# Performance work log

Measured on AMD Instinct MI355X. Metric: run time of the kernel, lower is better.

The kernel has to match this reference:

```python
import jax, jax.numpy as jnp
import numpy as np

S = 4          # number of species / per-species sub-modules
CUTOFF = 5.2


def _routed_mlp(feat, W, b, species_, activate=True):
    # Species-routed MLP: equivalent to per-species index_select -> m_i -> index_add.
    # Compute all species branches vectorized, then select with one-hot mask.
    h = jnp.einsum('ni,sio->nso', feat, W) + b            # [N, S, out]
    if activate:
        h = jax.nn.gelu(h)
    onehot = jax.nn.one_hot(species_, S, dtype=feat.dtype)  # [N, S]; -1 -> all-zero row
    return jnp.einsum('nso,ns->no', h, onehot)            # [N, out]


def _smooth_cutoff(d, rc):
    x = jnp.clip(d / rc, 0.0, 1.0 - 1e-6)
    f = jnp.exp(1.0 - 1.0 / (1.0 - x * x))
    return jnp.where(d < rc, f, 0.0)


def setup_inputs() -> dict:
    key = jax.random.key(0)
    ks = jax.random.split(key, 12)
    B, A, AEV, MO, NO, P = 256, 128, 1008, 256, 128, 262144
    N = B * A
    FIN = MO + NO  # 384
    species = jax.random.randint(ks[0], (B, A), 0, S, dtype=jnp.int32)
    aev = jax.random.normal(ks[1], (B, A, AEV), dtype=jnp.float32)
    atom_index12 = jax.random.randint(ks[2], (2, P), 0, N, dtype=jnp.int32)
    distances = jax.random.uniform(ks[3], (P,), dtype=jnp.float32) * CUTOFF
    total_charges = jax.random.randint(ks[4], (B,), -2, 3).astype(jnp.float32)

    def w(k, shape, fan_in):
        return jax.random.normal(k, shape, dtype=jnp.float32) / np.sqrt(fan_in)

    Wm0 = w(ks[5], (S, AEV, MO), AEV); bm0 = jnp.zeros((S, MO), jnp.float32)
    Wn0 = w(ks[6], (S, MO, NO), MO);   bn0 = jnp.zeros((S, NO), jnp.float32)
    Wm1 = w(ks[7], (S, FIN, MO), FIN); bm1 = jnp.zeros((S, MO), jnp.float32)
    Wn1 = w(ks[8], (S, MO, NO), MO);   bn1 = jnp.zeros((S, NO), jnp.float32)
    Wf  = w(ks[9], (S, FIN, 1), FIN);  bf  = jnp.zeros((S, 1), jnp.float32)
    return dict(species=species, aev=aev, atom_index12=atom_index12,
                distances=distances, total_charges=total_charges,
                Wm0=Wm0, bm0=bm0, Wn0=Wn0, bn0=bn0,
                Wm1=Wm1, bm1=bm1, Wn1=Wn1, bn1=bn1,
                Wf=Wf, bf=bf,
                factor=jnp.float32(1.0), prefactor=jnp.float32(1.0))


def reference(species, aev, atom_index12, distances, total_charges,
              Wm0, bm0, Wn0, bn0, Wm1, bm1, Wn1, bn1, Wf, bf,
              factor, prefactor):
    B, A = species.shape
    species_ = species.reshape(-1)                 # [N]
    feat = aev.reshape(-1, aev.shape[-1])          # [N, AEV]

    # ExpDistanceDecay * smooth cutoff, shared by every pass
    decay = (prefactor ** 2) * jnp.exp(-(factor ** 2) * distances) \
            * _smooth_cutoff(distances, CUTOFF)    # [P]
    idx_flat = atom_index12.reshape(-1)            # [2P] scatter targets
    idx_flip = atom_index12[::-1].reshape(-1)      # [2P] gather sources (flipud)
    decay2 = jnp.tile(decay, 2)                    # [2P]

    for (Wm, bm, Wn, bn) in ((Wm0, bm0, Wn0, bn0), (Wm1, bm1, Wn1, bn1)):
        internal = _routed_mlp(feat, Wm, bm, species_)     # [N, MO]
        neigh = _routed_mlp(internal, Wn, bn, species_)    # [N, NO]
        msgs = neigh[idx_flip] * decay2[:, None]           # [2P, NO]
        merged = jnp.zeros_like(neigh).at[idx_flat].add(msgs)
        feat = jnp.concatenate([internal, merged], axis=-1)  # [N, MO+NO]

    pre = _routed_mlp(feat, Wf, bf, species_, activate=False)[:, 0].reshape(B, A)

    dummy_mask = species != -1
    n_real = dummy_mask.sum(-1, keepdims=True).astype(pre.dtype)
    charges = pre + (total_charges - pre.sum(-1))[:, None] / n_real
    charges = jnp.where(dummy_mask, charges, 0.0)
    return species, charges, pre
```

## Files before the change

kernel.cpp:

```cpp
#include <hip/hip_runtime.h>
#include <hip/hip_bf16.h>
#include <math.h>

constexpr int S_  = 4;
constexpr int MO  = 256;
constexpr int NO  = 128;
constexpr int FIN = 384;
#define CUTOFF_F 5.2f

typedef short bf16x8 __attribute__((ext_vector_type(8)));
typedef float f32x16 __attribute__((ext_vector_type(16)));

__device__ __forceinline__ float gelu_tanh(float x) {
    float u = 0.7978845608028654f * (x + 0.044715f * x * x * x);
    return 0.5f * x * (1.0f + tanhf(u));
}
__device__ __forceinline__ unsigned short f2bf(float x) {
    unsigned u = __float_as_uint(x);
    u = (u + 0x7fffu + ((u >> 16) & 1u)) >> 16;
    return (unsigned short)u;
}
__device__ __forceinline__ float bf2f(unsigned short h) {
    return __uint_as_float(((unsigned)h) << 16);
}

__global__ void decay_kernel(const float* __restrict__ dist, const float* __restrict__ fa_,
                             const float* __restrict__ pf_, float* __restrict__ decay, int P) {
    int i = blockIdx.x * blockDim.x + threadIdx.x;
    if (i >= P) return;
    float fa = fa_[0], pf = pf_[0];
    float d = dist[i];
    float x = fminf(fmaxf(d / CUTOFF_F, 0.0f), 1.0f - 1e-6f);
    float f = expf(1.0f - 1.0f / (1.0f - x * x));
    float w = (d < CUTOFF_F) ? f : 0.0f;
    decay[i] = pf * pf * expf(-(fa * fa) * d) * w;
}

__global__ void species_hist(const int* __restrict__ sp, int* __restrict__ bhist, int N) {
    __shared__ int h[S_];
    int t = threadIdx.x, b = blockIdx.x;
    if (t < S_) h[t] = 0;
    __syncthreads();
    int i = b * 256 + t;
    if (i < N) {
        int s = sp[i];
        if (s >= 0 && s < S_) atomicAdd(&h[s], 1);
    }
    __syncthreads();
    if (t < S_) bhist[b * 4 + t] = h[t];
}
__global__ void species_scan(const int* __restrict__ bhist, int* __restrict__ cnt,
                             int* __restrict__ pbase, int nb) {
    if (threadIdx.x != 0) return;
    int tot[S_];
    for (int s = 0; s < S_; ++s) {
        int sum = 0;
        for (int b = 0; b < nb; ++b) sum += bhist[b * 4 + s];
        tot[s] = sum;
    }
    int off = 0;
    for (int s = 0; s < S_; ++s) { cnt[s] = tot[s]; cnt[4 + s] = off; off += tot[s]; }
    for (int s = 0; s < S_; ++s) {
        int run = cnt[4 + s];
        for (int b = 0; b < nb; ++b) { pbase[b * 4 + s] = run; run += bhist[b * 4 + s]; }
    }
}
__global__ void species_fill(const int* __restrict__ sp, const int* __restrict__ pbase,
                             int* __restrict__ perm, int N) {
    __shared__ int cur[S_];
    int t = threadIdx.x, b = blockIdx.x;
    if (t < S_) cur[t] = pbase[b * 4 + t];
    __syncthreads();
    int i = b * 256 + t;
    if (i < N) {
        int s = sp[i];
        if (s >= 0 && s < S_) {
            int pos = atomicAdd(&cur[s], 1);
            perm[pos] = i;
        }
    }
}

__global__ void edge_count(const int* __restrict__ ai, int* __restrict__ degree, int P2) {
    int e = blockIdx.x * blockDim.x + threadIdx.x;
    if (e < P2) atomicAdd(&degree[ai[e]], 1);
}
__global__ void scan_rowptr(const int* __restrict__ degree, int* __restrict__ rowptr,
                            int* __restrict__ cursor, int N) {
    __shared__ int lds[1024];
    int t = threadIdx.x;
    int per = N / 1024;
    int base = t * per;
    int sum = 0;
    for (int i = 0; i < per; ++i) sum += degree[base + i];
    lds[t] = sum;
    __syncthreads();
    int v = sum;
    for (int ofs = 1; ofs < 1024; ofs <<= 1) {
        int add = (t >= ofs) ? lds[t - ofs] : 0;
        __syncthreads();
        v += add;
        lds[t] = v;
        __syncthreads();
    }
    int run = v - sum;
    for (int i = 0; i < per; ++i) {
        int d = degree[base + i];
        rowptr[base + i] = run;
        cursor[base + i] = run;
        run += d;
    }
    if (t == 1023) rowptr[N] = run;
}
__global__ void edge_fill(const int* __restrict__ ai, const float* __restrict__ decay,
                          int* __restrict__ cursor, int* __restrict__ col,
                          float* __restrict__ wgt, int P) {
    int e = blockIdx.x * blockDim.x + threadIdx.x;
    if (e >= 2 * P) return;
    int p = (e < P) ? e : e - P;
    int dst = ai[e];
    int src = (e < P) ? ai[P + p] : ai[p];
    int pos = atomicAdd(&cursor[dst], 1);
    col[pos] = src;
    wgt[pos] = decay[p];
}

__global__ void cast_aev(const float* __restrict__ in, unsigned short* __restrict__ outb, int total4) {
    int i = blockIdx.x * blockDim.x + threadIdx.x;
    if (i >= total4) return;
    float4 v = ((const float4*)in)[i];
    ushort4 o; o.x = f2bf(v.x); o.y = f2bf(v.y); o.z = f2bf(v.z); o.w = f2bf(v.w);
    ((ushort4*)outb)[i] = o;
}

__global__ void transpose_cast(const float* __restrict__ W, unsigned short* __restrict__ Wt,
                               int K, int NC) {
    __shared__ float tile[32][33];
    int s = blockIdx.z;
    int nb = blockIdx.x * 32, kb = blockIdx.y * 32;
    int tx = threadIdx.x & 31, ty = threadIdx.x >> 5;
    const float* Wb = W + (size_t)s * K * NC;
    unsigned short* Wo = Wt + (size_t)s * NC * K;
#pragma unroll
    for (int i = 0; i < 4; ++i) {
        int k = kb + ty + i * 8;
        tile[ty + i * 8][tx] = (k < K) ? Wb[(size_t)k * NC + nb + tx] : 0.0f;
    }
    __syncthreads();
#pragma unroll
    for (int i = 0; i < 4; ++i) {
        int n = nb + ty + i * 8;
        int k = kb + tx;
        if (k < K) Wo[(size_t)n * K + k] = f2bf(tile[tx][ty + i * 8]);
    }
}

template<int K, int NC, bool ACT>
__launch_bounds__(256, 2)
__global__ void mfma_gemm(const unsigned short* __restrict__ A, int lda,
                          const unsigned short* __restrict__ Wt,
                          const float* __restrict__ bias,
                          unsigned short* __restrict__ C, int ldc,
                          const int* __restrict__ cnt, const int* __restrict__ perm) {
    const int s = blockIdx.z;
    const int count = cnt[s];
    const int row0 = blockIdx.y * 128;
    if (row0 >= count) return;
    const int off = cnt[4 + s];
    const int c0 = blockIdx.x * 128;

    __shared__ unsigned short As[128 * 40];
    __shared__ unsigned short Bs[128 * 40];
    __shared__ int rix[128];

    const int t = threadIdx.x;
    const int lane = t & 63, wave = t >> 6;
    const int wm = wave >> 1, wn = wave & 1;
    const int l31 = lane & 31, lhi = lane >> 5;

    if (t < 128) {
        int ri = row0 + t;
        rix[t] = (ri < count) ? perm[off + ri] : -1;
    }
    __syncthreads();

    const int r2 = t >> 1, half = t & 1;
    const int gA = rix[r2];
    const unsigned short* wrow = Wt + ((size_t)s * NC + c0 + r2) * K;

    f32x16 acc00 = {}, acc01 = {}, acc10 = {}, acc11 = {};
    const float4 zf4 = make_float4(0.f, 0.f, 0.f, 0.f);

    for (int k0 = 0; k0 < K; k0 += 32) {
        const int kk = k0 + half * 16;
        const bool v = (kk < K);
        float4 a0 = zf4, a1 = zf4, b0 = zf4, b1 = zf4;
        if (v) {
            if (gA >= 0) {
                const float4* p = (const float4*)(A + (size_t)gA * lda + kk);
                a0 = p[0]; a1 = p[1];
            }
            const float4* q = (const float4*)(wrow + kk);
            b0 = q[0]; b1 = q[1];
        }
        __syncthreads();
        *(float4*)(&As[r2 * 40 + half * 16])     = a0;
        *(float4*)(&As[r2 * 40 + half * 16 + 8]) = a1;
        *(float4*)(&Bs[r2 * 40 + half * 16])     = b0;
        *(float4*)(&Bs[r2 * 40 + half * 16 + 8]) = b1;
        __syncthreads();
#pragma unroll
        for (int ks = 0; ks < 2; ++ks) {
            const int ch = (ks * 2 + lhi) * 8;
            bf16x8 fa0 = *(const bf16x8*)(&As[(wm * 64 +  0 + l31) * 40 + ch]);
            bf16x8 fa1 = *(const bf16x8*)(&As[(wm * 64 + 32 + l31) * 40 + ch]);
            bf16x8 fb0 = *(const bf16x8*)(&Bs[(wn * 64 +  0 + l31) * 40 + ch]);
            bf16x8 fb1 = *(const bf16x8*)(&Bs[(wn * 64 + 32 + l31) * 40 + ch]);
            acc00 = __builtin_amdgcn_mfma_f32_32x32x16_bf16(fa0, fb0, acc00, 0, 0, 0);
            acc01 = __builtin_amdgcn_mfma_f32_32x32x16_bf16(fa0, fb1, acc01, 0, 0, 0);
            acc10 = __builtin_amdgcn_mfma_f32_32x32x16_bf16(fa1, fb0, acc10, 0, 0, 0);
            acc11 = __builtin_amdgcn_mfma_f32_32x32x16_bf16(fa1, fb1, acc11, 0, 0, 0);
        }
    }

    const float* bp = bias + s * NC;
    auto store = [&](const f32x16& vv, int fm, int fn) {
        int col = c0 + wn * 64 + fn * 32 + l31;
        float bia = bp[col];
#pragma unroll
        for (int reg = 0; reg < 16; ++reg) {
            int frow = (reg & 3) + 8 * (reg >> 2) + 4 * lhi;
            int r = wm * 64 + fm * 32 + frow;
            int g = rix[r];
            if (g >= 0) {
                float x = vv[reg] + bia;
                if (ACT) x = gelu_tanh(x);
                C[(size_t)g * ldc + col] = f2bf(x);
            }
        }
    };
    store(acc00, 0, 0); store(acc01, 0, 1); store(acc10, 1, 0); store(acc11, 1, 1);
}

template<int MODE>
__global__ void gather_rows(const unsigned short* __restrict__ neigh,
                            const int* __restrict__ rowptr, const int* __restrict__ col,
                            const float* __restrict__ wgt,
                            unsigned short* __restrict__ featout,
                            float* __restrict__ mergedout) {
    int row = blockIdx.x * 4 + (threadIdx.x >> 6);
    int lane = threadIdx.x & 63;
    int b = rowptr[row], e = rowptr[row + 1];
    int j = lane * 2;
    float a0 = 0.f, a1 = 0.f;
    for (int i = b; i < e; ++i) {
        int src = col[i];
        float w = wgt[i];
        unsigned pk = *(const unsigned*)(neigh + (size_t)src * NO + j);
        a0 += bf2f((unsigned short)(pk & 0xffffu)) * w;
        a1 += bf2f((unsigned short)(pk >> 16)) * w;
    }
    if (MODE == 0) {
        unsigned short o0 = f2bf(a0), o1 = f2bf(a1);
        *(unsigned*)(featout + (size_t)row * FIN + MO + j) = ((unsigned)o1 << 16) | (unsigned)o0;
    } else {
        float2 o; o.x = a0; o.y = a1;
        *(float2*)(mergedout + (size_t)row * NO + j) = o;
    }
}

__global__ void final_kernel(const unsigned short* __restrict__ int1, const float* __restrict__ merged,
                             const float* __restrict__ Wf, const float* __restrict__ bfb,
                             const int* __restrict__ species, float* __restrict__ out, int N) {
    int w = (int)((blockIdx.x * (size_t)blockDim.x + threadIdx.x) >> 6);
    int lane = threadIdx.x & 63;
    if (w >= N) return;
    int s = species[w];
    float acc = 0.0f;
    if (s >= 0) {
        const float* wp = Wf + (size_t)s * FIN;
        for (int k = lane; k < MO; k += 64) acc += bf2f(int1[(size_t)w * MO + k]) * wp[k];
        for (int k = lane; k < NO; k += 64) acc += merged[(size_t)w * NO + k] * wp[MO + k];
    }
    for (int o = 32; o > 0; o >>= 1) acc += __shfl_down(acc, o, 64);
    if (lane == 0) {
        float pre = (s >= 0) ? (acc + bfb[s]) : 0.0f;
        out[2 * (size_t)N + w] = pre;
        out[w] = (float)s;
    }
}

__global__ void charges_kernel(const float* __restrict__ pre_buf, const int* __restrict__ species,
                               const float* __restrict__ tc, float* __restrict__ out, int N, int A) {
    int b = blockIdx.x;
    int a = threadIdx.x;
    int idx = b * A + a;
    float pre = pre_buf[idx];
    int sp = species[idx];
    bool mask = (sp != -1);
    float v = pre;
    int c = mask ? 1 : 0;
    for (int o = 32; o > 0; o >>= 1) {
        v += __shfl_down(v, o, 64);
        c += __shfl_down(c, o, 64);
    }
    __shared__ float ssum[2];
    __shared__ int scnt[2];
    int wid = threadIdx.x >> 6;
    if ((threadIdx.x & 63) == 0) { ssum[wid] = v; scnt[wid] = c; }
    __syncthreads();
    float total = ssum[0] + ssum[1];
    int nreal = scnt[0] + scnt[1];
    float ch = pre + (tc[b] - total) / (float)max(nreal, 1);
    out[(size_t)N + idx] = mask ? ch : 0.0f;
}

extern "C" void kernel_launch(void* const* d_in, const int* in_sizes, int n_in,
                              void* d_out, int out_size, void* d_ws, size_t ws_size,
                              hipStream_t stream) {
    const int*   species = (const int*)d_in[0];
    const float* aev     = (const float*)d_in[1];
    const int*   ai      = (const int*)d_in[2];
    const float* dist    = (const float*)d_in[3];
    const float* tc      = (const float*)d_in[4];
    const float* Wm0 = (const float*)d_in[5];  const float* bm0 = (const float*)d_in[6];
    const float* Wn0 = (const float*)d_in[7];  const float* bn0 = (const float*)d_in[8];
    const float* Wm1 = (const float*)d_in[9];  const float* bm1 = (const float*)d_in[10];
    const float* Wn1 = (const float*)d_in[11]; const float* bn1 = (const float*)d_in[12];
    const float* Wf  = (const float*)d_in[13]; const float* bf  = (const float*)d_in[14];
    const float* factor    = (const float*)d_in[15];
    const float* prefactor = (const float*)d_in[16];

    const int N   = in_sizes[0];
    const int AEV = in_sizes[1] / N;
    const int P   = in_sizes[3];
    const int B   = in_sizes[4];
    const int A   = N / B;

    float* out = (float*)d_out;

    char* base = (char*)d_ws;
    size_t o = 0;
    auto take = [&](size_t bytes) -> char* {
        o = (o + 255) & ~(size_t)255;
        char* p = base + o; o += bytes; return p;
    };
    unsigned short* feat1_bf = (unsigned short*)take((size_t)N * FIN * 2);
    unsigned short* int1_bf  = (unsigned short*)take((size_t)N * MO * 2);
    char* region             = take((size_t)N * AEV * 2);
    unsigned short* aev_bf   = (unsigned short*)region;
    unsigned short* neigh_bf = (unsigned short*)region;
    size_t roff = ((size_t)N * NO * 2 + 255) & ~(size_t)255;
    float* merged_f = (float*)(region + roff);
    roff += (size_t)N * NO * 4;
    roff = (roff + 255) & ~(size_t)255;
    int* rowptr = (int*)(region + roff);  roff += (size_t)(N + 1) * 4; roff = (roff + 255) & ~(size_t)255;
    int* cursor = (int*)(region + roff);  roff += (size_t)N * 4;       roff = (roff + 255) & ~(size_t)255;
    int* degree = (int*)(region + roff);  roff += (size_t)N * 4;       roff = (roff + 255) & ~(size_t)255;
    int* ecol   = (int*)(region + roff);  roff += (size_t)2 * P * 4;   roff = (roff + 255) & ~(size_t)255;
    float* ewgt = (float*)(region + roff);
    float* decay = (float*)take((size_t)P * 4);
    unsigned short* Wm0t = (unsigned short*)take((size_t)S_ * MO * AEV * 2);
    unsigned short* Wn0t = (unsigned short*)take((size_t)S_ * NO * MO * 2);
    unsigned short* Wm1t = (unsigned short*)take((size_t)S_ * MO * FIN * 2);
    unsigned short* Wn1t = (unsigned short*)take((size_t)S_ * NO * MO * 2);
    int* perm  = (int*)take((size_t)N * 4);
    int* cnt   = (int*)take(64);
    const int nb = (N + 255) / 256;
    int* bhist = (int*)take((size_t)nb * 4 * 4);
    int* pbase = (int*)take((size_t)nb * 4 * 4);

    species_hist<<<nb, 256, 0, stream>>>(species, bhist, N);
    species_scan<<<1, 64, 0, stream>>>(bhist, cnt, pbase, nb);
    species_fill<<<nb, 256, 0, stream>>>(species, pbase, perm, N);
    decay_kernel<<<(P + 255) / 256, 256, 0, stream>>>(dist, factor, prefactor, decay, P);

    const int tot4 = N * (AEV / 4);
    cast_aev<<<(tot4 + 255) / 256, 256, 0, stream>>>(aev, aev_bf, tot4);
    transpose_cast<<<dim3(MO / 32, (AEV + 31) / 32, S_), 256, 0, stream>>>(Wm0, Wm0t, AEV, MO);
    transpose_cast<<<dim3(NO / 32, MO / 32, S_), 256, 0, stream>>>(Wn0, Wn0t, MO, NO);
    transpose_cast<<<dim3(MO / 32, FIN / 32, S_), 256, 0, stream>>>(Wm1, Wm1t, FIN, MO);
    transpose_cast<<<dim3(NO / 32, MO / 32, S_), 256, 0, stream>>>(Wn1, Wn1t, MO, NO);

    const int rb = (N + 127) / 128;

    mfma_gemm<1008, 256, true><<<dim3(2, rb, S_), 256, 0, stream>>>(
        aev_bf, AEV, Wm0t, bm0, feat1_bf, FIN, cnt, perm);

    hipMemsetAsync(degree, 0, (size_t)N * 4, stream);
    edge_count<<<(2 * P + 255) / 256, 256, 0, stream>>>(ai, degree, 2 * P);
    scan_rowptr<<<1, 1024, 0, stream>>>(degree, rowptr, cursor, N);
    edge_fill<<<(2 * P + 255) / 256, 256, 0, stream>>>(ai, decay, cursor, ecol, ewgt, P);

    mfma_gemm<256, 128, true><<<dim3(1, rb, S_), 256, 0, stream>>>(
        feat1_bf, FIN, Wn0t, bn0, neigh_bf, NO, cnt, perm);
    gather_rows<0><<<N / 4, 256, 0, stream>>>(neigh_bf, rowptr, ecol, ewgt, feat1_bf, nullptr);

    mfma_gemm<384, 256, true><<<dim3(2, rb, S_), 256, 0, stream>>>(
        feat1_bf, FIN, Wm1t, bm1, int1_bf, MO, cnt, perm);
    mfma_gemm<256, 128, true><<<dim3(1, rb, S_), 256, 0, stream>>>(
        int1_bf, MO, Wn1t, bn1, neigh_bf, NO, cnt, perm);
    gather_rows<1><<<N / 4, 256, 0, stream>>>(neigh_bf, rowptr, ecol, ewgt, nullptr, merged_f);

    final_kernel<<<(N * 64 + 255) / 256, 256, 0, stream>>>(
        int1_bf, merged_f, Wf, bf, species, out, N);
    charges_kernel<<<B, A, 0, stream>>>(out + 2 * (size_t)N, species, tc, out, N, A);
}
```

Measured before the change: 724.1 us.

## Fuse fp32 AEV cast into first GEMM and double-buffer shared tiles

```diff
diff --git a/kernel.cpp b/kernel.cpp
--- a/kernel.cpp
+++ b/kernel.cpp
@@ -125,14 +125,6 @@
     wgt[pos] = decay[p];
 }
 
-__global__ void cast_aev(const float* __restrict__ in, unsigned short* __restrict__ outb, int total4) {
-    int i = blockIdx.x * blockDim.x + threadIdx.x;
-    if (i >= total4) return;
-    float4 v = ((const float4*)in)[i];
-    ushort4 o; o.x = f2bf(v.x); o.y = f2bf(v.y); o.z = f2bf(v.z); o.w = f2bf(v.w);
-    ((ushort4*)outb)[i] = o;
-}
-
 __global__ void transpose_cast(const float* __restrict__ W, unsigned short* __restrict__ Wt,
                                int K, int NC) {
     __shared__ float tile[32][33];
@@ -155,9 +147,9 @@
     }
 }
 
-template<int K, int NC, bool ACT>
+template<int K, int NC, bool ACT, bool AF32>
 __launch_bounds__(256, 2)
-__global__ void mfma_gemm(const unsigned short* __restrict__ A, int lda,
+__global__ void mfma_gemm(const void* __restrict__ Aptr, int lda,
                           const unsigned short* __restrict__ Wt,
                           const float* __restrict__ bias,
                           unsigned short* __restrict__ C, int ldc,
@@ -169,8 +161,8 @@
     const int off = cnt[4 + s];
     const int c0 = blockIdx.x * 128;
 
-    __shared__ unsigned short As[128 * 40];
-    __shared__ unsigned short Bs[128 * 40];
+    __shared__ unsigned short As[2][128 * 40];
+    __shared__ unsigned short Bs[2][128 * 40];
     __shared__ int rix[128];
 
     const int t = threadIdx.x;
@@ -189,38 +181,79 @@
     const unsigned short* wrow = Wt + ((size_t)s * NC + c0 + r2) * K;
 
     f32x16 acc00 = {}, acc01 = {}, acc10 = {}, acc11 = {};
-    const float4 zf4 = make_float4(0.f, 0.f, 0.f, 0.f);
-
-    for (int k0 = 0; k0 < K; k0 += 32) {
-        const int kk = k0 + half * 16;
+
+    uint4 pa0 = {0,0,0,0}, pa1 = {0,0,0,0}, pb0 = {0,0,0,0}, pb1 = {0,0,0,0};
+    float4 fa0{}, fa1{}, fa2{}, fa3{};
+
+    auto prefetch = [&](int it) {
+        const int kk = it * 32 + half * 16;
         const bool v = (kk < K);
-        float4 a0 = zf4, a1 = zf4, b0 = zf4, b1 = zf4;
+        uint4 z = {0,0,0,0};
+        pb0 = z; pb1 = z;
         if (v) {
-            if (gA >= 0) {
-                const float4* p = (const float4*)(A + (size_t)gA * lda + kk);
-                a0 = p[0]; a1 = p[1];
+            const uint4* q = (const uint4*)(wrow + kk);
+            pb0 = q[0]; pb1 = q[1];
+        }
+        if (AF32) {
+            float4 zf = make_float4(0.f,0.f,0.f,0.f);
+            fa0 = zf; fa1 = zf; fa2 = zf; fa3 = zf;
+            if (v && gA >= 0) {
+                const float4* p = (const float4*)((const float*)Aptr + (size_t)gA * lda + kk);
+                fa0 = p[0]; fa1 = p[1]; fa2 = p[2]; fa3 = p[3];
             }
-            const float4* q = (const float4*)(wrow + kk);
-            b0 = q[0]; b1 = q[1];
-        }
+        } else {
+            pa0 = z; pa1 = z;
+            if (v && gA >= 0) {
+                const uint4* p = (const uint4*)((const unsigned short*)Aptr + (size_t)gA * lda + kk);
+                pa0 = p[0]; pa1 = p[1];
+            }
+        }
+    };
+    auto stage = [&](int buf) {
+        uint4 aw0, aw1;
+        if (AF32) {
+            union { unsigned short us[8]; uint4 v; } k0, k1;
+            const float* f0 = (const float*)&fa0;
+            const float* f1 = (const float*)&fa1;
+            const float* f2 = (const float*)&fa2;
+            const float* f3 = (const float*)&fa3;
+#pragma unroll
+            for (int i = 0; i < 4; ++i) { k0.us[i] = f2bf(f0[i]); k0.us[4 + i] = f2bf(f1[i]); }
+#pragma unroll
+            for (int i = 0; i < 4; ++i) { k1.us[i] = f2bf(f2[i]); k1.us[4 + i] = f2bf(f3[i]); }
+            aw0 = k0.v; aw1 = k1.v;
+        } else {
+            aw0 = pa0; aw1 = pa1;
+        }
+        *(uint4*)(&As[buf][r2 * 40 + half * 16])     = aw0;
+        *(uint4*)(&As[buf][r2 * 40 + half * 16 + 8]) = aw1;
+        *(uint4*)(&Bs[buf][r2 * 40 + half * 16])     = pb0;
+        *(uint4*)(&Bs[buf][r2 * 40 + half * 16 + 8]) = pb1;
+    };
+
+    const int NIT = (K + 31) / 32;
+    prefetch(0);
+    stage(0);
+    int cur = 0;
+
+    for (int it = 0; it < NIT; ++it) {
         __syncthreads();
-        *(float4*)(&As[r2 * 40 + half * 16])     = a0;
-        *(float4*)(&As[r2 * 40 + half * 16 + 8]) = a1;
-        *(float4*)(&Bs[r2 * 40 + half * 16])     = b0;
-        *(float4*)(&Bs[r2 * 40 + half * 16 + 8]) = b1;
-        __syncthreads();
+        const bool more = (it + 1 < NIT);
+        if (more) prefetch(it + 1);
 #pragma unroll
         for (int ks = 0; ks < 2; ++ks) {
             const int ch = (ks * 2 + lhi) * 8;
-            bf16x8 fa0 = *(const bf16x8*)(&As[(wm * 64 +  0 + l31) * 40 + ch]);
-            bf16x8 fa1 = *(const bf16x8*)(&As[(wm * 64 + 32 + l31) * 40 + ch]);
-            bf16x8 fb0 = *(const bf16x8*)(&Bs[(wn * 64 +  0 + l31) * 40 + ch]);
-            bf16x8 fb1 = *(const bf16x8*)(&Bs[(wn * 64 + 32 + l31) * 40 + ch]);
-            acc00 = __builtin_amdgcn_mfma_f32_32x32x16_bf16(fa0, fb0, acc00, 0, 0, 0);
-            acc01 = __builtin_amdgcn_mfma_f32_32x32x16_bf16(fa0, fb1, acc01, 0, 0, 0);
-            acc10 = __builtin_amdgcn_mfma_f32_32x32x16_bf16(fa1, fb0, acc10, 0, 0, 0);
-            acc11 = __builtin_amdgcn_mfma_f32_32x32x16_bf16(fa1, fb1, acc11, 0, 0, 0);
-        }
+            bf16x8 a0 = *(const bf16x8*)(&As[cur][(wm * 64 +  0 + l31) * 40 + ch]);
+            bf16x8 a1 = *(const bf16x8*)(&As[cur][(wm * 64 + 32 + l31) * 40 + ch]);
+            bf16x8 b0 = *(const bf16x8*)(&Bs[cur][(wn * 64 +  0 + l31) * 40 + ch]);
+            bf16x8 b1 = *(const bf16x8*)(&Bs[cur][(wn * 64 + 32 + l31) * 40 + ch]);
+            acc00 = __builtin_amdgcn_mfma_f32_32x32x16_bf16(a0, b0, acc00, 0, 0, 0);
+            acc01 = __builtin_amdgcn_mfma_f32_32x32x16_bf16(a0, b1, acc01, 0, 0, 0);
+            acc10 = __builtin_amdgcn_mfma_f32_32x32x16_bf16(a1, b0, acc10, 0, 0, 0);
+            acc11 = __builtin_amdgcn_mfma_f32_32x32x16_bf16(a1, b1, acc11, 0, 0, 0);
+        }
+        if (more) stage(cur ^ 1);
+        cur ^= 1;
     }
 
     const float* bp = bias + s * NC;
@@ -348,7 +381,6 @@
     unsigned short* feat1_bf = (unsigned short*)take((size_t)N * FIN * 2);
     unsigned short* int1_bf  = (unsigned short*)take((size_t)N * MO * 2);
     char* region             = take((size_t)N * AEV * 2);
-    unsigned short* aev_bf   = (unsigned short*)region;
     unsigned short* neigh_bf = (unsigned short*)region;
     size_t roff = ((size_t)N * NO * 2 + 255) & ~(size_t)255;
     float* merged_f = (float*)(region + roff);
@@ -375,8 +407,11 @@
     species_fill<<<nb, 256, 0, stream>>>(species, pbase, perm, N);
     decay_kernel<<<(P + 255) / 256, 256, 0, stream>>>(dist, factor, prefactor, decay, P);
 
-    const int tot4 = N * (AEV / 4);
-    cast_aev<<<(tot4 + 255) / 256, 256, 0, stream>>>(aev, aev_bf, tot4);
+    hipMemsetAsync(degree, 0, (size_t)N * 4, stream);
+    edge_count<<<(2 * P + 255) / 256, 256, 0, stream>>>(ai, degree, 2 * P);
+    scan_rowptr<<<1, 1024, 0, stream>>>(degree, rowptr, cursor, N);
+    edge_fill<<<(2 * P + 255) / 256, 256, 0, stream>>>(ai, decay, cursor, ecol, ewgt, P);
+
     transpose_cast<<<dim3(MO / 32, (AEV + 31) / 32, S_), 256, 0, stream>>>(Wm0, Wm0t, AEV, MO);
     transpose_cast<<<dim3(NO / 32, MO / 32, S_), 256, 0, stream>>>(Wn0, Wn0t, MO, NO);
     transpose_cast<<<dim3(MO / 32, FIN / 32, S_), 256, 0, stream>>>(Wm1, Wm1t, FIN, MO);
@@ -384,21 +419,15 @@
 
     const int rb = (N + 127) / 128;
 
-    mfma_gemm<1008, 256, true><<<dim3(2, rb, S_), 256, 0, stream>>>(
-        aev_bf, AEV, Wm0t, bm0, feat1_bf, FIN, cnt, perm);
-
-    hipMemsetAsync(degree, 0, (size_t)N * 4, stream);
-    edge_count<<<(2 * P + 255) / 256, 256, 0, stream>>>(ai, degree, 2 * P);
-    scan_rowptr<<<1, 1024, 0, stream>>>(degree, rowptr, cursor, N);
-    edge_fill<<<(2 * P + 255) / 256, 256, 0, stream>>>(ai, decay, cursor, ecol, ewgt, P);
-
-    mfma_gemm<256, 128, true><<<dim3(1, rb, S_), 256, 0, stream>>>(
+    mfma_gemm<1008, 256, true, true><<<dim3(2, rb, S_), 256, 0, stream>>>(
+        aev, AEV, Wm0t, bm0, feat1_bf, FIN, cnt, perm);
+    mfma_gemm<256, 128, true, false><<<dim3(1, rb, S_), 256, 0, stream>>>(
         feat1_bf, FIN, Wn0t, bn0, neigh_bf, NO, cnt, perm);
     gather_rows<0><<<N / 4, 256, 0, stream>>>(neigh_bf, rowptr, ecol, ewgt, feat1_bf, nullptr);
 
-    mfma_gemm<384, 256, true><<<dim3(2, rb, S_), 256, 0, stream>>>(
+    mfma_gemm<384, 256, true, false><<<dim3(2, rb, S_), 256, 0, stream>>>(
         feat1_bf, FIN, Wm1t, bm1, int1_bf, MO, cnt, perm);
-    mfma_gemm<256, 128, true><<<dim3(1, rb, S_), 256, 0, stream>>>(
+    mfma_gemm<256, 128, true, false><<<dim3(1, rb, S_), 256, 0, stream>>>(
         int1_bf, MO, Wn1t, bn1, neigh_bf, NO, cnt, perm);
     gather_rows<1><<<N / 4, 256, 0, stream>>>(neigh_bf, rowptr, ecol, ewgt, nullptr, merged_f);
 
```

After: 691.2 us. -4.5%, faster.

## Double-buffer LDS tiles with register prefetch and widen K step in MFMA GEMM

Applied to the files above, without the earlier changes.

```diff
diff --git a/kernel.cpp b/kernel.cpp
--- a/kernel.cpp
+++ b/kernel.cpp
@@ -154,6 +154,8 @@
         if (k < K) Wo[(size_t)n * K + k] = f2bf(tile[tx][ty + i * 8]);
     }
 }
+
+constexpr int LSTR = 72;
 
 template<int K, int NC, bool ACT>
 __launch_bounds__(256, 2)
@@ -169,8 +171,8 @@
     const int off = cnt[4 + s];
     const int c0 = blockIdx.x * 128;
 
-    __shared__ unsigned short As[128 * 40];
-    __shared__ unsigned short Bs[128 * 40];
+    __shared__ unsigned short As[2][128 * LSTR];
+    __shared__ unsigned short Bs[2][128 * LSTR];
     __shared__ int rix[128];
 
     const int t = threadIdx.x;
@@ -186,41 +188,58 @@
 
     const int r2 = t >> 1, half = t & 1;
     const int gA = rix[r2];
+    const unsigned short* Arow = (gA >= 0) ? (A + (size_t)gA * lda) : nullptr;
     const unsigned short* wrow = Wt + ((size_t)s * NC + c0 + r2) * K;
 
     f32x16 acc00 = {}, acc01 = {}, acc10 = {}, acc11 = {};
-    const float4 zf4 = make_float4(0.f, 0.f, 0.f, 0.f);
-
-    for (int k0 = 0; k0 < K; k0 += 32) {
-        const int kk = k0 + half * 16;
-        const bool v = (kk < K);
-        float4 a0 = zf4, a1 = zf4, b0 = zf4, b1 = zf4;
-        if (v) {
-            if (gA >= 0) {
-                const float4* p = (const float4*)(A + (size_t)gA * lda + kk);
-                a0 = p[0]; a1 = p[1];
+
+    uint4 pa[4], pb[4];
+    auto prefetch = [&](int it) {
+        const int kbase = it * 64 + half * 32;
+#pragma unroll
+        for (int q = 0; q < 4; ++q) {
+            const int kk = kbase + q * 8;
+            const bool v = (kk < K);
+            uint4 z = {0, 0, 0, 0};
+            pa[q] = z; pb[q] = z;
+            if (v) {
+                if (Arow) pa[q] = *(const uint4*)(Arow + kk);
+                pb[q] = *(const uint4*)(wrow + kk);
             }
-            const float4* q = (const float4*)(wrow + kk);
-            b0 = q[0]; b1 = q[1];
         }
+    };
+    auto stage = [&](int buf) {
+        const int base = r2 * LSTR + half * 32;
+#pragma unroll
+        for (int q = 0; q < 4; ++q) {
+            *(uint4*)(&As[buf][base + q * 8]) = pa[q];
+            *(uint4*)(&Bs[buf][base + q * 8]) = pb[q];
+        }
+    };
+
+    const int NIT = (K + 63) / 64;
+    prefetch(0);
+    stage(0);
+    int cur = 0;
+
+    for (int it = 0; it < NIT; ++it) {
         __syncthreads();
-        *(float4*)(&As[r2 * 40 + half * 16])     = a0;
-        *(float4*)(&As[r2 * 40 + half * 16 + 8]) = a1;
-        *(float4*)(&Bs[r2 * 40 + half * 16])     = b0;
-        *(float4*)(&Bs[r2 * 40 + half * 16 + 8]) = b1;
-        __syncthreads();
-#pragma unroll
-        for (int ks = 0; ks < 2; ++ks) {
+        const bool more = (it + 1 < NIT);
+        if (more) prefetch(it + 1);
+#pragma unroll
+        for (int ks = 0; ks < 4; ++ks) {
             const int ch = (ks * 2 + lhi) * 8;
-            bf16x8 fa0 = *(const bf16x8*)(&As[(wm * 64 +  0 + l31) * 40 + ch]);
-            bf16x8 fa1 = *(const bf16x8*)(&As[(wm * 64 + 32 + l31) * 40 + ch]);
-            bf16x8 fb0 = *(const bf16x8*)(&Bs[(wn * 64 +  0 + l31) * 40 + ch]);
-            bf16x8 fb1 = *(const bf16x8*)(&Bs[(wn * 64 + 32 + l31) * 40 + ch]);
-            acc00 = __builtin_amdgcn_mfma_f32_32x32x16_bf16(fa0, fb0, acc00, 0, 0, 0);
-            acc01 = __builtin_amdgcn_mfma_f32_32x32x16_bf16(fa0, fb1, acc01, 0, 0, 0);
-            acc10 = __builtin_amdgcn_mfma_f32_32x32x16_bf16(fa1, fb0, acc10, 0, 0, 0);
-            acc11 = __builtin_amdgcn_mfma_f32_32x32x16_bf16(fa1, fb1, acc11, 0, 0, 0);
+            bf16x8 a0 = *(const bf16x8*)(&As[cur][(wm * 64 +  0 + l31) * LSTR + ch]);
+            bf16x8 a1 = *(const bf16x8*)(&As[cur][(wm * 64 + 32 + l31) * LSTR + ch]);
+            bf16x8 b0 = *(const bf16x8*)(&Bs[cur][(wn * 64 +  0 + l31) * LSTR + ch]);
+            bf16x8 b1 = *(const bf16x8*)(&Bs[cur][(wn * 64 + 32 + l31) * LSTR + ch]);
+            acc00 = __builtin_amdgcn_mfma_f32_32x32x16_bf16(a0, b0, acc00, 0, 0, 0);
+            acc01 = __builtin_amdgcn_mfma_f32_32x32x16_bf16(a0, b1, acc01, 0, 0, 0);
+            acc10 = __builtin_amdgcn_mfma_f32_32x32x16_bf16(a1, b0, acc10, 0, 0, 0);
+            acc11 = __builtin_amdgcn_mfma_f32_32x32x16_bf16(a1, b1, acc11, 0, 0, 0);
         }
+        if (more) stage(cur ^ 1);
+        cur ^= 1;
     }
 
     const float* bp = bias + s * NC;
```

New measurement: 863.7 us. +19.3%, slower.

## Fuse second neighbor gather with final readout and unroll gather loops

Applied to the files above, without the earlier changes.

```diff
diff --git a/kernel.cpp b/kernel.cpp
--- a/kernel.cpp
+++ b/kernel.cpp
@@ -189,25 +189,25 @@
     const unsigned short* wrow = Wt + ((size_t)s * NC + c0 + r2) * K;
 
     f32x16 acc00 = {}, acc01 = {}, acc10 = {}, acc11 = {};
-    const float4 zf4 = make_float4(0.f, 0.f, 0.f, 0.f);
+    const uint4 z4 = {0, 0, 0, 0};
 
     for (int k0 = 0; k0 < K; k0 += 32) {
         const int kk = k0 + half * 16;
         const bool v = (kk < K);
-        float4 a0 = zf4, a1 = zf4, b0 = zf4, b1 = zf4;
+        uint4 a0 = z4, a1 = z4, b0 = z4, b1 = z4;
         if (v) {
             if (gA >= 0) {
-                const float4* p = (const float4*)(A + (size_t)gA * lda + kk);
+                const uint4* p = (const uint4*)(A + (size_t)gA * lda + kk);
                 a0 = p[0]; a1 = p[1];
             }
-            const float4* q = (const float4*)(wrow + kk);
+            const uint4* q = (const uint4*)(wrow + kk);
             b0 = q[0]; b1 = q[1];
         }
         __syncthreads();
-        *(float4*)(&As[r2 * 40 + half * 16])     = a0;
-        *(float4*)(&As[r2 * 40 + half * 16 + 8]) = a1;
-        *(float4*)(&Bs[r2 * 40 + half * 16])     = b0;
-        *(float4*)(&Bs[r2 * 40 + half * 16 + 8]) = b1;
+        *(uint4*)(&As[r2 * 40 + half * 16])     = a0;
+        *(uint4*)(&As[r2 * 40 + half * 16 + 8]) = a1;
+        *(uint4*)(&Bs[r2 * 40 + half * 16])     = b0;
+        *(uint4*)(&Bs[r2 * 40 + half * 16 + 8]) = b1;
         __syncthreads();
 #pragma unroll
         for (int ks = 0; ks < 2; ++ks) {
@@ -242,45 +242,77 @@
     store(acc00, 0, 0); store(acc01, 0, 1); store(acc10, 1, 0); store(acc11, 1, 1);
 }
 
-template<int MODE>
-__global__ void gather_rows(const unsigned short* __restrict__ neigh,
-                            const int* __restrict__ rowptr, const int* __restrict__ col,
-                            const float* __restrict__ wgt,
-                            unsigned short* __restrict__ featout,
-                            float* __restrict__ mergedout) {
+__global__ void gather_rows0(const unsigned short* __restrict__ neigh,
+                             const int* __restrict__ rowptr, const int* __restrict__ col,
+                             const float* __restrict__ wgt,
+                             unsigned short* __restrict__ featout) {
     int row = blockIdx.x * 4 + (threadIdx.x >> 6);
     int lane = threadIdx.x & 63;
     int b = rowptr[row], e = rowptr[row + 1];
     int j = lane * 2;
-    float a0 = 0.f, a1 = 0.f;
-    for (int i = b; i < e; ++i) {
-        int src = col[i];
-        float w = wgt[i];
-        unsigned pk = *(const unsigned*)(neigh + (size_t)src * NO + j);
-        a0 += bf2f((unsigned short)(pk & 0xffffu)) * w;
-        a1 += bf2f((unsigned short)(pk >> 16)) * w;
-    }
-    if (MODE == 0) {
-        unsigned short o0 = f2bf(a0), o1 = f2bf(a1);
-        *(unsigned*)(featout + (size_t)row * FIN + MO + j) = ((unsigned)o1 << 16) | (unsigned)o0;
-    } else {
-        float2 o; o.x = a0; o.y = a1;
-        *(float2*)(mergedout + (size_t)row * NO + j) = o;
-    }
-}
-
-__global__ void final_kernel(const unsigned short* __restrict__ int1, const float* __restrict__ merged,
+    float a0 = 0.f, a1 = 0.f, c0 = 0.f, c1 = 0.f;
+    int i = b;
+    for (; i + 1 < e; i += 2) {
+        int s0 = col[i], s1 = col[i + 1];
+        float w0 = wgt[i], w1 = wgt[i + 1];
+        unsigned p0 = *(const unsigned*)(neigh + (size_t)s0 * NO + j);
+        unsigned p1 = *(const unsigned*)(neigh + (size_t)s1 * NO + j);
+        a0 += bf2f((unsigned short)(p0 & 0xffffu)) * w0;
+        a1 += bf2f((unsigned short)(p0 >> 16)) * w0;
+        c0 += bf2f((unsigned short)(p1 & 0xffffu)) * w1;
+        c1 += bf2f((unsigned short)(p1 >> 16)) * w1;
+    }
+    if (i < e) {
+        int s0 = col[i];
+        float w0 = wgt[i];
+        unsigned p0 = *(const unsigned*)(neigh + (size_t)s0 * NO + j);
+        a0 += bf2f((unsigned short)(p0 & 0xffffu)) * w0;
+        a1 += bf2f((unsigned short)(p0 >> 16)) * w0;
+    }
+    a0 += c0; a1 += c1;
+    unsigned short o0 = f2bf(a0), o1 = f2bf(a1);
+    *(unsigned*)(featout + (size_t)row * FIN + MO + j) = ((unsigned)o1 << 16) | (unsigned)o0;
+}
+
+__global__ void gather_final(const unsigned short* __restrict__ neigh,
+                             const int* __restrict__ rowptr, const int* __restrict__ col,
+                             const float* __restrict__ wgt,
+                             const unsigned short* __restrict__ int1,
                              const float* __restrict__ Wf, const float* __restrict__ bfb,
                              const int* __restrict__ species, float* __restrict__ out, int N) {
-    int w = (int)((blockIdx.x * (size_t)blockDim.x + threadIdx.x) >> 6);
+    int w = blockIdx.x * 4 + (threadIdx.x >> 6);
     int lane = threadIdx.x & 63;
-    if (w >= N) return;
     int s = species[w];
     float acc = 0.0f;
     if (s >= 0) {
         const float* wp = Wf + (size_t)s * FIN;
-        for (int k = lane; k < MO; k += 64) acc += bf2f(int1[(size_t)w * MO + k]) * wp[k];
-        for (int k = lane; k < NO; k += 64) acc += merged[(size_t)w * NO + k] * wp[MO + k];
+        int b = rowptr[w], e = rowptr[w + 1];
+        int j = lane * 2;
+        float a0 = 0.f, a1 = 0.f, c0 = 0.f, c1 = 0.f;
+        int i = b;
+        for (; i + 1 < e; i += 2) {
+            int s0 = col[i], s1 = col[i + 1];
+            float w0 = wgt[i], w1 = wgt[i + 1];
+            unsigned p0 = *(const unsigned*)(neigh + (size_t)s0 * NO + j);
+            unsigned p1 = *(const unsigned*)(neigh + (size_t)s1 * NO + j);
+            a0 += bf2f((unsigned short)(p0 & 0xffffu)) * w0;
+            a1 += bf2f((unsigned short)(p0 >> 16)) * w0;
+            c0 += bf2f((unsigned short)(p1 & 0xffffu)) * w1;
+            c1 += bf2f((unsigned short)(p1 >> 16)) * w1;
+        }
+        if (i < e) {
+            int s0 = col[i];
+            float w0 = wgt[i];
+            unsigned p0 = *(const unsigned*)(neigh + (size_t)s0 * NO + j);
+            a0 += bf2f((unsigned short)(p0 & 0xffffu)) * w0;
+            a1 += bf2f((unsigned short)(p0 >> 16)) * w0;
+        }
+        a0 += c0; a1 += c1;
+        acc = a0 * wp[MO + j] + a1 * wp[MO + j + 1];
+        const unsigned short* ip = int1 + (size_t)w * MO + lane * 4;
+        ushort4 iv = *(const ushort4*)ip;
+        const float* wq = wp + lane * 4;
+        acc += bf2f(iv.x) * wq[0] + bf2f(iv.y) * wq[1] + bf2f(iv.z) * wq[2] + bf2f(iv.w) * wq[3];
     }
     for (int o = 32; o > 0; o >>= 1) acc += __shfl_down(acc, o, 64);
     if (lane == 0) {
@@ -351,9 +383,6 @@
     unsigned short* aev_bf   = (unsigned short*)region;
     unsigned short* neigh_bf = (unsigned short*)region;
     size_t roff = ((size_t)N * NO * 2 + 255) & ~(size_t)255;
-    float* merged_f = (float*)(region + roff);
-    roff += (size_t)N * NO * 4;
-    roff = (roff + 255) & ~(size_t)255;
     int* rowptr = (int*)(region + roff);  roff += (size_t)(N + 1) * 4; roff = (roff + 255) & ~(size_t)255;
     int* cursor = (int*)(region + roff);  roff += (size_t)N * 4;       roff = (roff + 255) & ~(size_t)255;
     int* degree = (int*)(region + roff);  roff += (size_t)N * 4;       roff = (roff + 255) & ~(size_t)255;
@@ -394,15 +423,14 @@
 
     mfma_gemm<256, 128, true><<<dim3(1, rb, S_), 256, 0, stream>>>(
         feat1_bf, FIN, Wn0t, bn0, neigh_bf, NO, cnt, perm);
-    gather_rows<0><<<N / 4, 256, 0, stream>>>(neigh_bf, rowptr, ecol, ewgt, feat1_bf, nullptr);
+    gather_rows0<<<N / 4, 256, 0, stream>>>(neigh_bf, rowptr, ecol, ewgt, feat1_bf);
 
     mfma_gemm<384, 256, true><<<dim3(2, rb, S_), 256, 0, stream>>>(
         feat1_bf, FIN, Wm1t, bm1, int1_bf, MO, cnt, perm);
     mfma_gemm<256, 128, true><<<dim3(1, rb, S_), 256, 0, stream>>>(
         int1_bf, MO, Wn1t, bn1, neigh_bf, NO, cnt, perm);
-    gather_rows<1><<<N / 4, 256, 0, stream>>>(neigh_bf, rowptr, ecol, ewgt, nullptr, merged_f);
-
-    final_kernel<<<(N * 64 + 255) / 256, 256, 0, stream>>>(
-        int1_bf, merged_f, Wf, bf, species, out, N);
+
+    gather_final<<<N / 4, 256, 0, stream>>>(
+        neigh_bf, rowptr, ecol, ewgt, int1_bf, Wf, bf, species, out, N);
     charges_kernel<<<B, A, 0, stream>>>(out + 2 * (size_t)N, species, tc, out, N, A);
 }
```

Measured after the change: 673.5 us. 1.08x faster.
